# Kernel optimization log

Hardware: AMD Instinct MI355X
Metric: run time of the kernel (lower is better)

The kernel has to match this reference:

```python
import jax, jax.numpy as jnp
import numpy as np

ITEM_NUM = 100000
EMBED = 128
HIDDEN = 256
BETA = 0.5
B, H = 2048, 200


def setup_inputs() -> dict:
    key = jax.random.key(0)
    ks = jax.random.split(key, 10)
    history = jax.random.randint(ks[0], (B, H), 0, ITEM_NUM)
    target = jax.random.randint(ks[1], (B,), 0, ITEM_NUM)
    history_region = jax.random.randint(ks[2], (B, H), 0, 64)
    target_region = jax.random.randint(ks[3], (B,), 0, 64)
    # scaled small since forward multiplies by 1000 before sigmoid
    target_distance = jax.random.uniform(ks[4], (B, H, 2), dtype=jnp.float32) * 1e-3
    embed_history = 0.01 * jax.random.normal(ks[5], (ITEM_NUM, EMBED), dtype=jnp.float32)
    embed_target = 0.01 * jax.random.normal(ks[6], (ITEM_NUM, EMBED), dtype=jnp.float32)
    W1 = 0.05 * jax.random.normal(ks[7], (EMBED + 2, HIDDEN), dtype=jnp.float32)
    b1 = jnp.zeros((HIDDEN,), dtype=jnp.float32)
    W2 = 0.05 * jax.random.normal(ks[8], (HIDDEN, 1), dtype=jnp.float32)
    Wd = 0.5 * jax.random.normal(ks[9], (2, 2), dtype=jnp.float32)
    bd = jnp.zeros((2,), dtype=jnp.float32)
    return {"history": history, "target": target, "history_region": history_region,
            "target_region": target_region, "target_distance": target_distance,
            "embed_history": embed_history, "embed_target": embed_target,
            "W1": W1, "b1": b1, "W2": W2, "Wd": Wd, "bd": bd}


def reference(history, target, history_region, target_region, target_distance,
              embed_history, embed_target, W1, b1, W2, Wd, bd):
    h = embed_history[history]                 # [B,H,d]
    t = embed_target[target]                   # [B,d]
    # dist_layer: sigmoid(Linear(2,2)(1000 * lat_long))
    dist = jax.nn.sigmoid((target_distance * 1000.0) @ Wd + bd)   # [B,H,2]
    inp = jnp.concatenate([h * t[:, None, :], dist], axis=-1)     # [B,H,d+2]
    attn = jax.nn.relu(inp @ W1 + b1) @ W2                        # [B,H,1]
    mask = (history != target[:, None]).astype(h.dtype)
    exp_A = jnp.exp(attn[..., 0]) * mask                          # [B,H]
    exp_sum = jnp.sum(exp_A, axis=-1, keepdims=True) ** BETA      # [B,1]
    w = exp_A / exp_sum                                           # [B,H]
    pred = jnp.einsum('bhd,bh,bd->b', h, w, t)                    # [B]
    return jax.nn.sigmoid(pred)
```

## Files before the change

### kernel.cpp

```cpp
#include <hip/hip_runtime.h>
#include <hip/hip_bf16.h>

#define B_SZ 2048
#define H_SZ 200
#define BH (B_SZ * H_SZ)
#define EMB 128
#define HID 256
#define KP 160
#define LDA 168
#define BM 64

typedef short bf16x8 __attribute__((ext_vector_type(8)));
typedef float f32x4 __attribute__((ext_vector_type(4)));

__device__ __forceinline__ unsigned short bfc(float x) {
    unsigned u = __float_as_uint(x);
    u += 0x7FFFu + ((u >> 16) & 1u);
    return (unsigned short)(u >> 16);
}
__device__ __forceinline__ float bf2f(unsigned short h) {
    return __uint_as_float(((unsigned)h) << 16);
}

__global__ void prep_w1t(const float* __restrict__ W1, unsigned short* __restrict__ W1T) {
    int i = blockIdx.x * 256 + threadIdx.x;
    int n = i / KP;
    int k = i - n * KP;
    float v = (k < 130) ? W1[k * HID + n] : 0.f;
    W1T[i] = bfc(v);
}

__global__ void prep_ehb(const float* __restrict__ eh, unsigned short* __restrict__ ehb) {
    size_t t = (size_t)blockIdx.x * 256 + threadIdx.x;
    const float4* src = (const float4*)eh + t * 2;
    float4 a = src[0], b = src[1];
    uint4 o;
    o.x = (unsigned)bfc(a.x) | ((unsigned)bfc(a.y) << 16);
    o.y = (unsigned)bfc(a.z) | ((unsigned)bfc(a.w) << 16);
    o.z = (unsigned)bfc(b.x) | ((unsigned)bfc(b.y) << 16);
    o.w = (unsigned)bfc(b.z) | ((unsigned)bfc(b.w) << 16);
    ((uint4*)ehb)[t] = o;
}

template<bool BF16E>
__global__ __launch_bounds__(512, 4) void attn_kernel(
    const int* __restrict__ history, const int* __restrict__ target,
    const float* __restrict__ td, const float* __restrict__ eh,
    const unsigned short* __restrict__ ehb,
    const float* __restrict__ et, const unsigned short* __restrict__ W1T,
    const float* __restrict__ b1, const float* __restrict__ W2,
    const float* __restrict__ Wd, const float* __restrict__ bd,
    float* __restrict__ expA, float* __restrict__ uOut)
{
    __shared__ __align__(16) unsigned short At[BM * LDA];
    __shared__ float u_lds[BM];
    __shared__ float red[BM][8];

    const int tid = threadIdx.x;
    const int rowBase = blockIdx.x * BM;

    {
        const int m = tid >> 3;
        const int o = tid & 7;
        const int row = rowBase + m;
        const int b = row / H_SZ;
        const int idx = history[row];
        const int tgt = target[b];

        float hv[16];
        if (BF16E) {
            const bf16x8* hp = (const bf16x8*)(ehb + (size_t)idx * EMB + o * 16);
            bf16x8 h0 = hp[0], h1 = hp[1];
#pragma unroll
            for (int i = 0; i < 8; ++i) {
                hv[i]     = bf2f((unsigned short)h0[i]);
                hv[8 + i] = bf2f((unsigned short)h1[i]);
            }
        } else {
            const float4* hp = (const float4*)(eh + (size_t)idx * EMB + o * 16);
            float4 a0 = hp[0], a1 = hp[1], a2 = hp[2], a3 = hp[3];
            hv[0]=a0.x; hv[1]=a0.y; hv[2]=a0.z; hv[3]=a0.w;
            hv[4]=a1.x; hv[5]=a1.y; hv[6]=a1.z; hv[7]=a1.w;
            hv[8]=a2.x; hv[9]=a2.y; hv[10]=a2.z; hv[11]=a2.w;
            hv[12]=a3.x; hv[13]=a3.y; hv[14]=a3.z; hv[15]=a3.w;
        }
        const float4* tp = (const float4*)(et + (size_t)tgt * EMB + o * 16);
        float4 t0 = tp[0], t1 = tp[1], t2 = tp[2], t3 = tp[3];
        float tv[16] = {t0.x,t0.y,t0.z,t0.w, t1.x,t1.y,t1.z,t1.w,
                        t2.x,t2.y,t2.z,t2.w, t3.x,t3.y,t3.z,t3.w};

        float su = 0.f;
        unsigned pk[8];
#pragma unroll
        for (int i = 0; i < 8; ++i) {
            float p0 = hv[2*i] * tv[2*i];
            float p1 = hv[2*i+1] * tv[2*i+1];
            su += p0 + p1;
            pk[i] = (unsigned)bfc(p0) | ((unsigned)bfc(p1) << 16);
        }
        uint4* dst = (uint4*)(At + m * LDA + o * 16);
        dst[0] = make_uint4(pk[0], pk[1], pk[2], pk[3]);
        dst[1] = make_uint4(pk[4], pk[5], pk[6], pk[7]);

        su += __shfl_xor(su, 1);
        su += __shfl_xor(su, 2);
        su += __shfl_xor(su, 4);
        if (o == 0) {
            u_lds[m] = su;
            float x0 = td[(size_t)row * 2 + 0] * 1000.f;
            float x1 = td[(size_t)row * 2 + 1] * 1000.f;
            float d0 = x0 * Wd[0] + x1 * Wd[2] + bd[0];
            float d1 = x0 * Wd[1] + x1 * Wd[3] + bd[1];
            d0 = 1.f / (1.f + expf(-d0));
            d1 = 1.f / (1.f + expf(-d1));
            At[m * LDA + 128] = bfc(d0);
            At[m * LDA + 129] = bfc(d1);
        } else if (o == 1) {
            unsigned* z = (unsigned*)(At + m * LDA + 130);
#pragma unroll
            for (int k = 0; k < 15; ++k) z[k] = 0;
        }
    }
    __syncthreads();

    const int l  = tid & 63;
    const int w  = tid >> 6;
    const int lr = l & 15;
    const int lq = l >> 4;

    float b1v[2], w2v[2];
#pragma unroll
    for (int nt = 0; nt < 2; ++nt) {
        const int n = w * 32 + nt * 16 + lr;
        b1v[nt] = b1[n];
        w2v[nt] = W2[n];
    }

    f32x4 acc[4][2];
#pragma unroll
    for (int mt = 0; mt < 4; ++mt)
#pragma unroll
        for (int nt = 0; nt < 2; ++nt)
            acc[mt][nt] = (f32x4){0.f, 0.f, 0.f, 0.f};

#pragma unroll
    for (int ks = 0; ks < 5; ++ks) {
        bf16x8 bfr[2];
#pragma unroll
        for (int nt = 0; nt < 2; ++nt)
            bfr[nt] = *reinterpret_cast<const bf16x8*>(
                W1T + (w * 32 + nt * 16 + lr) * KP + ks * 32 + lq * 8);
#pragma unroll
        for (int mt = 0; mt < 4; ++mt) {
            bf16x8 af = *reinterpret_cast<const bf16x8*>(
                At + (mt * 16 + lr) * LDA + ks * 32 + lq * 8);
#pragma unroll
            for (int nt = 0; nt < 2; ++nt)
                acc[mt][nt] = __builtin_amdgcn_mfma_f32_16x16x32_bf16(
                    af, bfr[nt], acc[mt][nt], 0, 0, 0);
        }
    }

#pragma unroll
    for (int mt = 0; mt < 4; ++mt) {
#pragma unroll
        for (int r = 0; r < 4; ++r) {
            float s = 0.f;
#pragma unroll
            for (int nt = 0; nt < 2; ++nt) {
                float hvv = acc[mt][nt][r] + b1v[nt];
                hvv = fmaxf(hvv, 0.f);
                s += hvv * w2v[nt];
            }
            s += __shfl_xor(s, 1);
            s += __shfl_xor(s, 2);
            s += __shfl_xor(s, 4);
            s += __shfl_xor(s, 8);
            if (lr == 0) red[mt * 16 + lq * 4 + r][w] = s;
        }
    }
    __syncthreads();

    if (tid < BM) {
        const int row = rowBase + tid;
        const int b = row / H_SZ;
        float attn = 0.f;
#pragma unroll
        for (int ww = 0; ww < 8; ++ww) attn += red[tid][ww];
        float e = (history[row] != target[b]) ? expf(attn) : 0.f;
        expA[row] = e;
        uOut[row] = u_lds[tid];
    }
}

__global__ void finalize_kernel(const float* __restrict__ expA,
                                const float* __restrict__ uIn,
                                float* __restrict__ out)
{
    const int l = threadIdx.x & 63;
    const int w = threadIdx.x >> 6;
    const int b = blockIdx.x * 4 + w;
    const float* ea = expA + b * H_SZ;
    const float* uu = uIn + b * H_SZ;
    float se = 0.f, su = 0.f;
    for (int h = l; h < H_SZ; h += 64) {
        float e = ea[h];
        se += e;
        su += e * uu[h];
    }
#pragma unroll
    for (int off = 32; off; off >>= 1) {
        se += __shfl_xor(se, off);
        su += __shfl_xor(su, off);
    }
    if (l == 0) {
        float pred = su / sqrtf(se);
        out[b] = 1.f / (1.f + expf(-pred));
    }
}

extern "C" void kernel_launch(void* const* d_in, const int* in_sizes, int n_in,
                              void* d_out, int out_size, void* d_ws, size_t ws_size,
                              hipStream_t stream) {
    const int*   history = (const int*)d_in[0];
    const int*   target  = (const int*)d_in[1];
    const float* td      = (const float*)d_in[4];
    const float* eh      = (const float*)d_in[5];
    const float* et      = (const float*)d_in[6];
    const float* W1      = (const float*)d_in[7];
    const float* b1      = (const float*)d_in[8];
    const float* W2      = (const float*)d_in[9];
    const float* Wd      = (const float*)d_in[10];
    const float* bd      = (const float*)d_in[11];
    float* out = (float*)d_out;

    char* ws = (char*)d_ws;
    unsigned short* W1T = (unsigned short*)ws;
    float* expA = (float*)(ws + 81920);
    float* u    = (float*)(ws + 81920 + 1638400);
    unsigned short* ehb = (unsigned short*)(ws + 81920 + 2 * 1638400);
    const size_t need_bf16 = 81920 + 2ull * 1638400 + 25600000ull;
    const bool useBf16 = ws_size >= need_bf16;

    prep_w1t<<<KP * HID / 256, 256, 0, stream>>>(W1, W1T);
    if (useBf16) {
        prep_ehb<<<1600000 / 256, 256, 0, stream>>>(eh, ehb);
        attn_kernel<true><<<BH / BM, 512, 0, stream>>>(history, target, td, eh, ehb,
                                                       et, W1T, b1, W2, Wd, bd, expA, u);
    } else {
        attn_kernel<false><<<BH / BM, 512, 0, stream>>>(history, target, td, eh, ehb,
                                                        et, W1T, b1, W2, Wd, bd, expA, u);
    }
    finalize_kernel<<<B_SZ / 4, 256, 0, stream>>>(expA, u, out);
}
```

Before: 121.2 us.

## Fuse attention and finalize into one block-per-batch kernel with async LDS loads

Each block now handles one batch row (200 history items). It folds the target embedding into the W1 weights so the raw bf16 history rows can be loaded straight into swizzled LDS with global_load_lds, pipelined across four tiles. The distance features are applied as a rank-2 epilogue correction instead of extra K columns, and the softmax/weighted-sum finalize is done in-block, which removes the expA/u intermediate buffers and the separate finalize launch. This changes rounding (bf16 of W1*t rather than bf16 of h*t), drops the fp32 fallback path when the workspace is small, and the last tile leaves most of its 64 rows unused.

New measurement: 109.8 us. -9.4%, faster.

```diff
diff --git a/kernel.cpp b/kernel.cpp
--- a/kernel.cpp
+++ b/kernel.cpp
@@ -3,15 +3,15 @@
 
 #define B_SZ 2048
 #define H_SZ 200
-#define BH (B_SZ * H_SZ)
 #define EMB 128
 #define HID 256
-#define KP 160
-#define LDA 168
-#define BM 64
 
 typedef short bf16x8 __attribute__((ext_vector_type(8)));
 typedef float f32x4 __attribute__((ext_vector_type(4)));
+
+#define WAIT_VM(n) asm volatile("s_waitcnt vmcnt(" #n ")" ::: "memory")
+#define WAIT_LGKM  asm volatile("s_waitcnt lgkmcnt(0)" ::: "memory")
+#define BAR        asm volatile("s_barrier" ::: "memory")
 
 __device__ __forceinline__ unsigned short bfc(float x) {
     unsigned u = __float_as_uint(x);
@@ -22,12 +22,11 @@
     return __uint_as_float(((unsigned)h) << 16);
 }
 
-__global__ void prep_w1t(const float* __restrict__ W1, unsigned short* __restrict__ W1T) {
+__global__ void prep_w1t(const float* __restrict__ W1, unsigned short* __restrict__ W1TB) {
     int i = blockIdx.x * 256 + threadIdx.x;
-    int n = i / KP;
-    int k = i - n * KP;
-    float v = (k < 130) ? W1[k * HID + n] : 0.f;
-    W1T[i] = bfc(v);
+    int n = i >> 7;
+    int k = i & 127;
+    W1TB[i] = bfc(W1[k * HID + n]);
 }
 
 __global__ void prep_ehb(const float* __restrict__ eh, unsigned short* __restrict__ ehb) {
@@ -42,180 +41,185 @@
     ((uint4*)ehb)[t] = o;
 }
 
-template<bool BF16E>
+__device__ __forceinline__ void gld_lds16(const unsigned short* g, unsigned short* l) {
+    __builtin_amdgcn_global_load_lds(
+        (const __attribute__((address_space(1))) void*)(g),
+        (__attribute__((address_space(3))) void*)(l),
+        16, 0, 0);
+}
+
 __global__ __launch_bounds__(512, 4) void attn_kernel(
     const int* __restrict__ history, const int* __restrict__ target,
-    const float* __restrict__ td, const float* __restrict__ eh,
-    const unsigned short* __restrict__ ehb,
-    const float* __restrict__ et, const unsigned short* __restrict__ W1T,
+    const float* __restrict__ td, const unsigned short* __restrict__ ehb,
+    const float* __restrict__ et, const unsigned short* __restrict__ W1TB,
     const float* __restrict__ b1, const float* __restrict__ W2,
-    const float* __restrict__ Wd, const float* __restrict__ bd,
-    float* __restrict__ expA, float* __restrict__ uOut)
+    const float* __restrict__ W1, const float* __restrict__ Wd,
+    const float* __restrict__ bd, float* __restrict__ out)
 {
-    __shared__ __align__(16) unsigned short At[BM * LDA];
-    __shared__ float u_lds[BM];
-    __shared__ float red[BM][8];
+    __shared__ __align__(16) unsigned short Abuf[4][64][128];
+    __shared__ float red[4][64][9];
+    __shared__ float2 dpack[256];
+    __shared__ int idxs[256];
+    __shared__ float t_f32[EMB];
+    __shared__ float finred[16];
 
     const int tid = threadIdx.x;
-    const int rowBase = blockIdx.x * BM;
-
+    const int b   = blockIdx.x;
+    const int tgt = target[b];
+
+    if (tid < 128) t_f32[tid] = et[(size_t)tgt * EMB + tid];
     {
-        const int m = tid >> 3;
-        const int o = tid & 7;
-        const int row = rowBase + m;
-        const int b = row / H_SZ;
-        const int idx = history[row];
-        const int tgt = target[b];
-
-        float hv[16];
-        if (BF16E) {
-            const bf16x8* hp = (const bf16x8*)(ehb + (size_t)idx * EMB + o * 16);
-            bf16x8 h0 = hp[0], h1 = hp[1];
-#pragma unroll
-            for (int i = 0; i < 8; ++i) {
-                hv[i]     = bf2f((unsigned short)h0[i]);
-                hv[8 + i] = bf2f((unsigned short)h1[i]);
-            }
-        } else {
-            const float4* hp = (const float4*)(eh + (size_t)idx * EMB + o * 16);
-            float4 a0 = hp[0], a1 = hp[1], a2 = hp[2], a3 = hp[3];
-            hv[0]=a0.x; hv[1]=a0.y; hv[2]=a0.z; hv[3]=a0.w;
-            hv[4]=a1.x; hv[5]=a1.y; hv[6]=a1.z; hv[7]=a1.w;
-            hv[8]=a2.x; hv[9]=a2.y; hv[10]=a2.z; hv[11]=a2.w;
-            hv[12]=a3.x; hv[13]=a3.y; hv[14]=a3.z; hv[15]=a3.w;
-        }
-        const float4* tp = (const float4*)(et + (size_t)tgt * EMB + o * 16);
-        float4 t0 = tp[0], t1 = tp[1], t2 = tp[2], t3 = tp[3];
-        float tv[16] = {t0.x,t0.y,t0.z,t0.w, t1.x,t1.y,t1.z,t1.w,
-                        t2.x,t2.y,t2.z,t2.w, t3.x,t3.y,t3.z,t3.w};
-
-        float su = 0.f;
-        unsigned pk[8];
-#pragma unroll
-        for (int i = 0; i < 8; ++i) {
-            float p0 = hv[2*i] * tv[2*i];
-            float p1 = hv[2*i+1] * tv[2*i+1];
-            su += p0 + p1;
-            pk[i] = (unsigned)bfc(p0) | ((unsigned)bfc(p1) << 16);
-        }
-        uint4* dst = (uint4*)(At + m * LDA + o * 16);
-        dst[0] = make_uint4(pk[0], pk[1], pk[2], pk[3]);
-        dst[1] = make_uint4(pk[4], pk[5], pk[6], pk[7]);
-
-        su += __shfl_xor(su, 1);
-        su += __shfl_xor(su, 2);
-        su += __shfl_xor(su, 4);
-        if (o == 0) {
-            u_lds[m] = su;
+        const int m0 = tid - 128;
+        if (m0 >= 0 && m0 < H_SZ) {
+            const int row = b * H_SZ + m0;
+            idxs[m0] = history[row];
             float x0 = td[(size_t)row * 2 + 0] * 1000.f;
             float x1 = td[(size_t)row * 2 + 1] * 1000.f;
             float d0 = x0 * Wd[0] + x1 * Wd[2] + bd[0];
             float d1 = x0 * Wd[1] + x1 * Wd[3] + bd[1];
             d0 = 1.f / (1.f + expf(-d0));
             d1 = 1.f / (1.f + expf(-d1));
-            At[m * LDA + 128] = bfc(d0);
-            At[m * LDA + 129] = bfc(d1);
-        } else if (o == 1) {
-            unsigned* z = (unsigned*)(At + m * LDA + 130);
-#pragma unroll
-            for (int k = 0; k < 15; ++k) z[k] = 0;
-        }
-    }
-    __syncthreads();
+            dpack[m0] = make_float2(d0, d1);
+        } else if (m0 >= H_SZ && m0 < 128 + 128) {
+            if (m0 < 256) dpack[m0] = make_float2(0.f, 0.f);
+        }
+    }
+    WAIT_LGKM; BAR;
 
     const int l  = tid & 63;
     const int w  = tid >> 6;
     const int lr = l & 15;
     const int lq = l >> 4;
 
-    float b1v[2], w2v[2];
+    bf16x8 bfrB[2][4];
+    float b1v[2], w2v[2], wd0[2], wd1[2];
 #pragma unroll
     for (int nt = 0; nt < 2; ++nt) {
         const int n = w * 32 + nt * 16 + lr;
         b1v[nt] = b1[n];
         w2v[nt] = W2[n];
-    }
-
-    f32x4 acc[4][2];
-#pragma unroll
-    for (int mt = 0; mt < 4; ++mt)
-#pragma unroll
-        for (int nt = 0; nt < 2; ++nt)
-            acc[mt][nt] = (f32x4){0.f, 0.f, 0.f, 0.f};
-
-#pragma unroll
-    for (int ks = 0; ks < 5; ++ks) {
-        bf16x8 bfr[2];
-#pragma unroll
-        for (int nt = 0; nt < 2; ++nt)
-            bfr[nt] = *reinterpret_cast<const bf16x8*>(
-                W1T + (w * 32 + nt * 16 + lr) * KP + ks * 32 + lq * 8);
-#pragma unroll
-        for (int mt = 0; mt < 4; ++mt) {
-            bf16x8 af = *reinterpret_cast<const bf16x8*>(
-                At + (mt * 16 + lr) * LDA + ks * 32 + lq * 8);
+        wd0[nt] = W1[128 * HID + n];
+        wd1[nt] = W1[129 * HID + n];
+#pragma unroll
+        for (int ks = 0; ks < 4; ++ks) {
+            const int k0 = ks * 32 + lq * 8;
+            bf16x8 wv = *reinterpret_cast<const bf16x8*>(W1TB + n * EMB + k0);
+            bf16x8 o;
+#pragma unroll
+            for (int j = 0; j < 8; ++j) {
+                float f = bf2f((unsigned short)wv[j]) * t_f32[k0 + j];
+                o[j] = (short)bfc(f);
+            }
+            bfrB[nt][ks] = o;
+        }
+    }
+
+    WAIT_VM(0);
+
+#pragma unroll
+    for (int t = 0; t < 3; ++t) {
+#pragma unroll
+        for (int j = 0; j < 2; ++j) {
+            const int rd = w * 8 + j * 4 + (l >> 4);
+            const int cc = (l & 15) ^ (rd & 7);
+            const unsigned short* g = ehb + (size_t)idxs[t * 64 + rd] * EMB + cc * 8;
+            gld_lds16(g, &Abuf[t][w * 8 + j * 4][0]);
+        }
+    }
+#pragma unroll
+    for (int j = 0; j < 2; ++j) {
+        const int rd = j * 4 + (l >> 4);
+        const int cc = (l & 15) ^ (rd & 7);
+        const unsigned short* g = ehb + (size_t)idxs[192 + rd] * EMB + cc * 8;
+        gld_lds16(g, &Abuf[3][j * 4][0]);
+    }
+
+#pragma unroll
+    for (int t = 0; t < 4; ++t) {
+        if (t == 0)      WAIT_VM(6);
+        else if (t == 1) WAIT_VM(4);
+        else if (t == 2) WAIT_VM(2);
+        else             WAIT_VM(0);
+        WAIT_LGKM;
+        BAR;
+
+        const int mc = (t == 3) ? 1 : 4;
+        const unsigned short* A = &Abuf[t][0][0];
+
+        f32x4 acc[4][2];
+#pragma unroll
+        for (int mt = 0; mt < 4; ++mt)
 #pragma unroll
             for (int nt = 0; nt < 2; ++nt)
-                acc[mt][nt] = __builtin_amdgcn_mfma_f32_16x16x32_bf16(
-                    af, bfr[nt], acc[mt][nt], 0, 0, 0);
-        }
-    }
-
-#pragma unroll
-    for (int mt = 0; mt < 4; ++mt) {
-#pragma unroll
-        for (int r = 0; r < 4; ++r) {
-            float s = 0.f;
-#pragma unroll
-            for (int nt = 0; nt < 2; ++nt) {
-                float hvv = acc[mt][nt][r] + b1v[nt];
-                hvv = fmaxf(hvv, 0.f);
-                s += hvv * w2v[nt];
+                acc[mt][nt] = (f32x4){0.f, 0.f, 0.f, 0.f};
+
+#pragma unroll
+        for (int ks = 0; ks < 4; ++ks) {
+#pragma unroll
+            for (int mt = 0; mt < 4; ++mt) if (mt < mc) {
+                const int ar = mt * 16 + lr;
+                const bf16x8 af = *reinterpret_cast<const bf16x8*>(
+                    A + ar * EMB + (((ks * 4 + lq) ^ (ar & 7)) * 8));
+                acc[mt][0] = __builtin_amdgcn_mfma_f32_16x16x32_bf16(af, bfrB[0][ks], acc[mt][0], 0, 0, 0);
+                acc[mt][1] = __builtin_amdgcn_mfma_f32_16x16x32_bf16(af, bfrB[1][ks], acc[mt][1], 0, 0, 0);
             }
-            s += __shfl_xor(s, 1);
-            s += __shfl_xor(s, 2);
-            s += __shfl_xor(s, 4);
-            s += __shfl_xor(s, 8);
-            if (lr == 0) red[mt * 16 + lq * 4 + r][w] = s;
-        }
-    }
-    __syncthreads();
-
-    if (tid < BM) {
-        const int row = rowBase + tid;
-        const int b = row / H_SZ;
+        }
+
+#pragma unroll
+        for (int mt = 0; mt < 4; ++mt) if (mt < mc) {
+#pragma unroll
+            for (int r = 0; r < 4; ++r) {
+                const int mrow = mt * 16 + lq * 4 + r;
+                float2 d = dpack[t * 64 + mrow];
+                float s = 0.f;
+#pragma unroll
+                for (int nt = 0; nt < 2; ++nt) {
+                    float hv = acc[mt][nt][r] + b1v[nt] + d.x * wd0[nt] + d.y * wd1[nt];
+                    hv = fmaxf(hv, 0.f);
+                    s += hv * w2v[nt];
+                }
+                s += __shfl_xor(s, 1);
+                s += __shfl_xor(s, 2);
+                s += __shfl_xor(s, 4);
+                s += __shfl_xor(s, 8);
+                if (lr == 0) red[t][mrow][w] = s;
+            }
+        }
+    }
+
+    WAIT_LGKM; BAR;
+
+    float se = 0.f, su = 0.f;
+    if (tid < H_SZ) {
+        const int tt = tid >> 6, mrow = tid & 63;
         float attn = 0.f;
 #pragma unroll
-        for (int ww = 0; ww < 8; ++ww) attn += red[tid][ww];
-        float e = (history[row] != target[b]) ? expf(attn) : 0.f;
-        expA[row] = e;
-        uOut[row] = u_lds[tid];
-    }
-}
-
-__global__ void finalize_kernel(const float* __restrict__ expA,
-                                const float* __restrict__ uIn,
-                                float* __restrict__ out)
-{
-    const int l = threadIdx.x & 63;
-    const int w = threadIdx.x >> 6;
-    const int b = blockIdx.x * 4 + w;
-    const float* ea = expA + b * H_SZ;
-    const float* uu = uIn + b * H_SZ;
-    float se = 0.f, su = 0.f;
-    for (int h = l; h < H_SZ; h += 64) {
-        float e = ea[h];
-        se += e;
-        su += e * uu[h];
-    }
-#pragma unroll
-    for (int off = 32; off; off >>= 1) {
+        for (int ww = 0; ww < 8; ++ww) attn += red[tt][mrow][ww];
+        const unsigned short* Arow = &Abuf[tt][mrow][0];
+        float u = 0.f;
+#pragma unroll
+        for (int c = 0; c < 16; ++c) {
+            bf16x8 hv = *reinterpret_cast<const bf16x8*>(Arow + ((c ^ (mrow & 7)) * 8));
+#pragma unroll
+            for (int j = 0; j < 8; ++j)
+                u += bf2f((unsigned short)hv[j]) * t_f32[c * 8 + j];
+        }
+        float e = (idxs[tid] != tgt) ? expf(attn) : 0.f;
+        se = e;
+        su = e * u;
+    }
+#pragma unroll
+    for (int off = 1; off < 64; off <<= 1) {
         se += __shfl_xor(se, off);
         su += __shfl_xor(su, off);
     }
-    if (l == 0) {
-        float pred = su / sqrtf(se);
-        out[b] = 1.f / (1.f + expf(-pred));
+    if (l == 0) { finred[w * 2] = se; finred[w * 2 + 1] = su; }
+    WAIT_LGKM; BAR;
+    if (tid == 0) {
+        float SE = 0.f, SU = 0.f;
+#pragma unroll
+        for (int ww = 0; ww < 8; ++ww) { SE += finred[2 * ww]; SU += finred[2 * ww + 1]; }
+        out[b] = 1.f / (1.f + expf(-SU / sqrtf(SE)));
     }
 }
 
@@ -235,21 +239,11 @@
     float* out = (float*)d_out;
 
     char* ws = (char*)d_ws;
-    unsigned short* W1T = (unsigned short*)ws;
-    float* expA = (float*)(ws + 81920);
-    float* u    = (float*)(ws + 81920 + 1638400);
-    unsigned short* ehb = (unsigned short*)(ws + 81920 + 2 * 1638400);
-    const size_t need_bf16 = 81920 + 2ull * 1638400 + 25600000ull;
-    const bool useBf16 = ws_size >= need_bf16;
-
-    prep_w1t<<<KP * HID / 256, 256, 0, stream>>>(W1, W1T);
-    if (useBf16) {
-        prep_ehb<<<1600000 / 256, 256, 0, stream>>>(eh, ehb);
-        attn_kernel<true><<<BH / BM, 512, 0, stream>>>(history, target, td, eh, ehb,
-                                                       et, W1T, b1, W2, Wd, bd, expA, u);
-    } else {
-        attn_kernel<false><<<BH / BM, 512, 0, stream>>>(history, target, td, eh, ehb,
-                                                        et, W1T, b1, W2, Wd, bd, expA, u);
-    }
-    finalize_kernel<<<B_SZ / 4, 256, 0, stream>>>(expA, u, out);
-}
+    unsigned short* W1TB = (unsigned short*)ws;
+    unsigned short* ehb  = (unsigned short*)(ws + 65536);
+
+    prep_w1t<<<HID * EMB / 256, 256, 0, stream>>>(W1, W1TB);
+    prep_ehb<<<1600000 / 256, 256, 0, stream>>>(eh, ehb);
+    attn_kernel<<<B_SZ, 512, 0, stream>>>(history, target, td, ehb, et, W1TB,
+                                          b1, W2, W1, Wd, bd, out);
+}
```
